# Optimization experiments

Hardware: AMD Instinct MI355X
Metric: run time of the kernel (lower is better)

The kernel has to match this reference:

```python
import jax, jax.numpy as jnp
import numpy as np

B, T, G, M, D = 8, 2048, 2, 1024, 256
ALPHA = -1.0      # config['dist_to_logits_alpha']
TAU = 2.0         # curr_temp = max_temp at init
EPS = 1e-10


def setup_inputs() -> dict:
    key = jax.random.key(0)
    k1, k2, k3 = jax.random.split(key, 3)
    x = jax.random.normal(k1, (B, T, G * D), dtype=jnp.float32)
    # nn.init.uniform_(embedding, -0.999, 0.999)
    embedding = jax.random.uniform(k2, (G, M, D), dtype=jnp.float32, minval=-0.999, maxval=0.999)
    # uniform noise for gumbel sampling, clipped away from {0,1}
    gumbel_u = jax.random.uniform(k3, (B * T, G, M), dtype=jnp.float32, minval=1e-6, maxval=1.0 - 1e-6)
    return {"x": x, "embedding": embedding, "gumbel_u": gumbel_u}


def reference(x, embedding, gumbel_u):
    b, t, c = x.shape
    g, m, d = embedding.shape
    xf = x.reshape(-1, g, d)                                  # [N, G, D]

    sq_e = jnp.sum(embedding ** 2, axis=-1)                   # [G, M]
    sq_x = jnp.sum(xf ** 2, axis=-1, keepdims=True)           # [N, G, 1]
    cross = jnp.einsum('ngd,gmd->ngm', xf, embedding)         # [N, G, M]
    logits = ALPHA * (sq_e[None] + sq_x - 2.0 * cross)        # [N, G, M]

    # hard-assignment code perplexity
    hard_x = jax.nn.one_hot(jnp.argmax(logits, axis=-1), m, dtype=logits.dtype)
    hard_probs = hard_x.mean(axis=0)                          # [G, M]
    code_perplexity = -jnp.sum(hard_probs * jnp.log2(hard_probs + EPS), axis=-1)

    # soft-assignment prob perplexity
    avg_probs = jax.nn.softmax(logits, axis=-1).mean(axis=0)  # [G, M]
    prob_perplexity = -jnp.sum(avg_probs * jnp.log2(avg_probs + EPS), axis=-1)

    # gumbel-softmax (hard=True, straight-through)
    gumbels = -jnp.log(-jnp.log(gumbel_u))
    y_soft = jax.nn.softmax((logits + gumbels) / TAU, axis=-1)
    idx = jnp.argmax(y_soft, axis=-1)                         # [N, G]
    y_hard = jax.nn.one_hot(idx, m, dtype=y_soft.dtype)
    st = y_hard + y_soft - jax.lax.stop_gradient(y_soft)      # straight-through one-hot

    # weighted sum over the codebook (avoids [N, G, M, D] blowup of the original)
    quantized = jnp.einsum('ngm,gmd->ngd', st, embedding).reshape(b, t, c)

    quantization_inds = idx.reshape(b, t, g).astype(jnp.int32)
    # use_vq_loss=True: F.mse_loss(x, quantized.detach())
    commitment_loss = jnp.mean((x - jax.lax.stop_gradient(quantized)) ** 2)

    return quantized, code_perplexity, prob_perplexity, quantization_inds, commitment_loss
```

## Files before the change

### kernel.cpp

```cpp
#include <hip/hip_runtime.h>
#include <math.h>

#define NTOT 16384
#define GG 2
#define MM 1024
#define DD 256

#define OFF_Q  ((size_t)0)
#define OFF_CP ((size_t)8388608)
#define OFF_PP ((size_t)8388610)
#define OFF_I  ((size_t)8388612)
#define OFF_L  ((size_t)8421380)

#define SHIFT 40.0f
#define REFINE_GAP 0.03f

typedef __attribute__((ext_vector_type(8))) short bf16x8;
typedef __attribute__((ext_vector_type(4))) float f32x4;
typedef unsigned short u16;
typedef unsigned int u32;

__device__ inline float wave_sum_f(float v) {
#pragma unroll
  for (int o = 32; o > 0; o >>= 1) v += __shfl_xor(v, o);
  return v;
}
__device__ inline u16 f2bf(float f) {
  u32 u = __float_as_uint(f);
  return (u16)((u + 0x7fffu + ((u >> 16) & 1u)) >> 16);
}
__device__ inline float bf2f(u16 h) {
  return __uint_as_float(((u32)h) << 16);
}
__device__ inline void async16(const void* g, void* l) {
  __builtin_amdgcn_global_load_lds(
      (const __attribute__((address_space(1))) u32*)g,
      (__attribute__((address_space(3))) u32*)l, 16, 0, 0);
}

#define WS_INVZ   32768
#define WS_EHSW   163840
#define WS_ELSW   1212416
#define WS_EST    2260992
#define WS_NEED3  (2260992ull + 2ull * MM * (size_t)NTOT * GG)

__global__ void vq_init2(const float* __restrict__ emb, float* __restrict__ sq_e,
                         float* __restrict__ avg, int* __restrict__ hist,
                         double* __restrict__ loss, u16* __restrict__ eh,
                         u16* __restrict__ el, int do_split) {
  const int row = blockIdx.x * 4 + (threadIdx.x >> 6);
  const int lane = threadIdx.x & 63;
  float4 e4 = *(const float4*)&emb[(size_t)row * DD + lane * 4];
  float s = e4.x * e4.x + e4.y * e4.y + e4.z * e4.z + e4.w * e4.w;
  s = wave_sum_f(s);
  if (do_split) {
    ushort4 h, l;
    h.x = f2bf(e4.x); l.x = f2bf(e4.x - bf2f(h.x));
    h.y = f2bf(e4.y); l.y = f2bf(e4.y - bf2f(h.y));
    h.z = f2bf(e4.z); l.z = f2bf(e4.z - bf2f(h.z));
    h.w = f2bf(e4.w); l.w = f2bf(e4.w - bf2f(h.w));
    *(ushort4*)&eh[(size_t)row * DD + lane * 4] = h;
    *(ushort4*)&el[(size_t)row * DD + lane * 4] = l;
  }
  if (lane == 0) sq_e[row] = s;
  if (blockIdx.x == 0) {
    for (int i = threadIdx.x; i < GG * MM; i += 256) { avg[i] = 0.f; hist[i] = 0; }
    if (threadIdx.x == 0) *loss = 0.0;
  }
}

__global__ void vq_init_swz(const float* __restrict__ emb, u16* __restrict__ eh_sw,
                            u16* __restrict__ el_sw) {
  int tid = blockIdx.x * 256 + threadIdx.x;
  int g = tid >> 15, rem = tid & 32767;
  int col = rem >> 5, kc = rem & 31;
  const float* src = emb + ((size_t)(g * MM + col)) * DD + kc * 8;
  float4 fa = *(const float4*)src;
  float4 fb = *(const float4*)(src + 4);
  float f[8] = {fa.x, fa.y, fa.z, fa.w, fb.x, fb.y, fb.z, fb.w};
  u16 hi[8], lo[8];
#pragma unroll
  for (int j = 0; j < 8; ++j) {
    hi[j] = f2bf(f[j]);
    lo[j] = f2bf(f[j] - bf2f(hi[j]));
  }
  int ct = col >> 6, cg = (col >> 4) & 3, l15 = col & 15;
  int ks = kc >> 2, quad = kc & 3;
  size_t chunk = ((((size_t)g * 16 + ct) * 8 + ks) * 4 + cg) * 64 + quad * 16 + l15;
  ushort4* dh = (ushort4*)(eh_sw + chunk * 8);
  ushort4* dl = (ushort4*)(el_sw + chunk * 8);
  dh[0] = make_ushort4(hi[0], hi[1], hi[2], hi[3]);
  dh[1] = make_ushort4(hi[4], hi[5], hi[6], hi[7]);
  dl[0] = make_ushort4(lo[0], lo[1], lo[2], lo[3]);
  dl[1] = make_ushort4(lo[4], lo[5], lo[6], lo[7]);
}

__global__ __launch_bounds__(256, 2) void vq_main3(
    const float* __restrict__ x, const float* __restrict__ emb,
    const float* __restrict__ gum, const float* __restrict__ sq_e,
    const u16* __restrict__ eh_sw, const u16* __restrict__ el_sw,
    float* __restrict__ out, u16* __restrict__ est, float* __restrict__ invZ_ws,
    int* __restrict__ hist, double* __restrict__ loss) {
  __shared__ u16 bt[2][32768];
  __shared__ int fidx_lds[128];

  const int g = blockIdx.y;
  const int n0 = blockIdx.x * 128;
  const int t = threadIdx.x;
  const int wave = t >> 6, lane = t & 63;
  const int quad = lane >> 4, l15 = lane & 15;
  const int nw = n0 + wave * 32;

  float* xs = (float*)&bt[0][0];
  {
    const float* xb = x + (size_t)nw * (GG * DD) + (size_t)g * DD;
#pragma unroll 4
    for (int j = 0; j < 32; ++j) {
      float4 v = *(const float4*)(xb + (size_t)j * (GG * DD) + lane * 4);
      *(float4*)&xs[wave * 8192 + j * 256 + ((lane ^ (j & 7)) << 2)] = v;
    }
  }
  __syncthreads();

  bf16x8 ah[2][8], al[2][8];
#pragma unroll
  for (int s = 0; s < 2; ++s) {
#pragma unroll
    for (int ks = 0; ks < 8; ++ks) {
      int row = s * 16 + l15;
      int c0 = ks * 8 + quad * 2;
      const float* base = &xs[wave * 8192 + row * 256];
      float4 f0 = *(const float4*)&base[((c0 ^ (row & 7)) << 2)];
      float4 f1 = *(const float4*)&base[(((c0 + 1) ^ (row & 7)) << 2)];
      float f[8] = {f0.x, f0.y, f0.z, f0.w, f1.x, f1.y, f1.z, f1.w};
#pragma unroll
      for (int j = 0; j < 8; ++j) {
        u16 h = f2bf(f[j]);
        ah[s][ks][j] = (short)h;
        al[s][ks][j] = (short)f2bf(f[j] - bf2f(h));
      }
    }
  }
  __syncthreads();

  const u16* sgh = eh_sw + (size_t)g * 16 * 16384;
  const u16* sgl = el_sw + (size_t)g * 16 * 16384;

  auto stage = [&](int ct, int buf) {
    const u16* sh = sgh + (size_t)ct * 16384;
    const u16* sl = sgl + (size_t)ct * 16384;
    u16* dh = &bt[buf][0];
    u16* dl = &bt[buf][16384];
#pragma unroll
    for (int j = 0; j < 8; ++j) {
      int slot = j * 4 + wave;
      async16(sh + slot * 512 + lane * 8, dh + slot * 512);
      async16(sl + slot * 512 + lane * 8, dl + slot * 512);
    }
  };

  float Zl[8], hv[8], z1[8], z2[8];
  int hid[8], i1[8], i2[8];
#pragma unroll
  for (int i = 0; i < 8; ++i) {
    Zl[i] = 0.f; hv[i] = -INFINITY; z1[i] = -INFINITY; z2[i] = -INFINITY;
    hid[i] = 0; i1[i] = 0; i2[i] = 0;
  }

  stage(0, 0);

#pragma unroll 1
  for (int ct = 0; ct < 16; ++ct) {
    __syncthreads();
    if (ct < 15) stage(ct + 1, (ct + 1) & 1);
    const u16* bh_p = &bt[ct & 1][0];
    const u16* bl_p = &bt[ct & 1][16384];
#pragma unroll 1
    for (int cg = 0; cg < 4; ++cg) {
      const int colG = ct * 64 + cg * 16 + l15;
      float sqv = sq_e[g * MM + colG];
      float gv[8];
#pragma unroll
      for (int s = 0; s < 2; ++s)
#pragma unroll
        for (int r = 0; r < 4; ++r)
          gv[s * 4 + r] =
              gum[((size_t)(nw + s * 16 + quad * 4 + r) * GG + g) * MM + colG];

      f32x4 c00 = {0,0,0,0}, c01 = {0,0,0,0}, c02 = {0,0,0,0};
      f32x4 c10 = {0,0,0,0}, c11 = {0,0,0,0}, c12 = {0,0,0,0};
#pragma unroll
      for (int ks = 0; ks < 8; ++ks) {
        int off = ((ks * 4 + cg) * 64 + lane) * 8;
        bf16x8 bh = *(const bf16x8*)(bh_p + off);
        bf16x8 bl = *(const bf16x8*)(bl_p + off);
        c00 = __builtin_amdgcn_mfma_f32_16x16x32_bf16(ah[0][ks], bh, c00, 0, 0, 0);
        c01 = __builtin_amdgcn_mfma_f32_16x16x32_bf16(ah[0][ks], bl, c01, 0, 0, 0);
        c02 = __builtin_amdgcn_mfma_f32_16x16x32_bf16(al[0][ks], bh, c02, 0, 0, 0);
        c10 = __builtin_amdgcn_mfma_f32_16x16x32_bf16(ah[1][ks], bh, c10, 0, 0, 0);
        c11 = __builtin_amdgcn_mfma_f32_16x16x32_bf16(ah[1][ks], bl, c11, 0, 0, 0);
        c12 = __builtin_amdgcn_mfma_f32_16x16x32_bf16(al[1][ks], bh, c12, 0, 0, 0);
      }
#pragma unroll
      for (int s = 0; s < 2; ++s) {
        const f32x4& a0 = s ? c10 : c00;
        const f32x4& a1 = s ? c11 : c01;
        const f32x4& a2 = s ? c12 : c02;
        ushort4 pk;
        u16* pp = (u16*)&pk;
#pragma unroll
        for (int r = 0; r < 4; ++r) {
          float lp = 2.f * (a0[r] + a1[r] + a2[r]) - sqv + SHIFT;
          float ev = expf(fminf(lp, 80.f));
          Zl[s * 4 + r] += ev;
          pp[r] = f2bf(ev);
          if (lp > hv[s * 4 + r]) { hv[s * 4 + r] = lp; hid[s * 4 + r] = colG; }
          float zz = lp - logf(-logf(gv[s * 4 + r]));
          if (zz > z1[s * 4 + r]) {
            z2[s * 4 + r] = z1[s * 4 + r]; i2[s * 4 + r] = i1[s * 4 + r];
            z1[s * 4 + r] = zz; i1[s * 4 + r] = colG;
          } else if (zz > z2[s * 4 + r]) {
            z2[s * 4 + r] = zz; i2[s * 4 + r] = colG;
          }
        }
        *(ushort4*)&est[((size_t)(g * MM + colG) << 14) + nw + s * 16 + quad * 4] = pk;
      }
    }
  }

#pragma unroll 1
  for (int s = 0; s < 2; ++s) {
#pragma unroll 1
    for (int r = 0; r < 4; ++r) {
      const int idx = s * 4 + r;
      const int row = wave * 32 + s * 16 + quad * 4 + r;
      const int n = n0 + row;
      float Zr = Zl[idx], hvr = hv[idx];
      int hir = hid[idx];
      float v1 = z1[idx], v2 = z2[idx];
      int j1 = i1[idx], j2 = i2[idx];
#pragma unroll
      for (int o = 1; o <= 8; o <<= 1) {
        Zr += __shfl_xor(Zr, o);
        float ohv = __shfl_xor(hvr, o); int ohi = __shfl_xor(hir, o);
        if (ohv > hvr || (ohv == hvr && ohi < hir)) { hvr = ohv; hir = ohi; }
        float w1 = __shfl_xor(v1, o), w2 = __shfl_xor(v2, o);
        int k1 = __shfl_xor(j1, o), k2 = __shfl_xor(j2, o);
        if (w1 > v1 || (w1 == v1 && k1 < j1)) {
          if (v1 > w2 || (v1 == w2 && j1 < k2)) { v2 = v1; j2 = j1; }
          else { v2 = w2; j2 = k2; }
          v1 = w1; j1 = k1;
        } else if (w1 > v2 || (w1 == v2 && k1 < j2)) { v2 = w1; j2 = k1; }
      }
      int fidx = j1;
      if (v1 - v2 < REFINE_GAP) {
        const float* xrow = x + (size_t)n * (GG * DD) + (size_t)g * DD;
        const float* eA = emb + ((size_t)g * MM + j1) * DD;
        const float* eB = emb + ((size_t)g * MM + j2) * DD;
        double dA = 0, sA = 0, dB = 0, sB = 0;
#pragma unroll
        for (int k = 0; k < 16; ++k) {
          int d = l15 * 16 + k;
          double xv = (double)xrow[d];
          double ea = (double)eA[d], eb = (double)eB[d];
          dA += xv * ea; sA += ea * ea;
          dB += xv * eb; sB += eb * eb;
        }
#pragma unroll
        for (int o = 1; o <= 8; o <<= 1) {
          dA += __shfl_xor(dA, o); sA += __shfl_xor(sA, o);
          dB += __shfl_xor(dB, o); sB += __shfl_xor(sB, o);
        }
        double uA = (double)gum[((size_t)n * GG + g) * MM + j1];
        double uB = (double)gum[((size_t)n * GG + g) * MM + j2];
        double zA = 2.0 * dA - sA - log(-log(uA));
        double zB = 2.0 * dB - sB - log(-log(uB));
        if (zB > zA || (zB == zA && j2 < j1)) fidx = j2;
      }
      if (l15 == 0) {
        out[OFF_I + (size_t)n * GG + g] = (float)fidx;
        atomicAdd(&hist[g * MM + hir], 1);
        invZ_ws[g * NTOT + n] = 1.f / Zr;
        fidx_lds[row] = fidx;
      }
    }
  }
  __syncthreads();

  {
    float ls = 0.f;
#pragma unroll 4
    for (int j = 0; j < 32; ++j) {
      int idx = j * 256 + t;
      int row = idx >> 6, f4 = idx & 63;
      int n = n0 + row, fi = fidx_lds[row];
      float4 e4 = *(const float4*)&emb[((size_t)g * MM + fi) * DD + f4 * 4];
      float4 x4 = *(const float4*)&x[(size_t)n * (GG * DD) + (size_t)g * DD + f4 * 4];
      *(float4*)&out[OFF_Q + (size_t)n * (GG * DD) + (size_t)g * DD + f4 * 4] = e4;
      float dx = x4.x - e4.x, dy = x4.y - e4.y, dz = x4.z - e4.z, dw = x4.w - e4.w;
      ls += dx * dx + dy * dy + dz * dz + dw * dw;
    }
    ls = wave_sum_f(ls);
    if (lane == 0) atomicAdd(loss, (double)ls);
  }
}

__global__ void vq_avg(const u16* __restrict__ est, const float* __restrict__ invZ,
                       float* __restrict__ avg) {
  int wid = blockIdx.x * 4 + (threadIdx.x >> 6);
  int lane = threadIdx.x & 63;
  const u16* base = est + ((size_t)wid << 14);
  const float* zp = invZ + ((wid >> 10) << 14);
  float acc = 0.f;
#pragma unroll 4
  for (int it = 0; it < 64; ++it) {
    int n = it * 256 + lane * 4;
    ushort4 e4 = *(const ushort4*)(base + n);
    float4 z4 = *(const float4*)(zp + n);
    acc += bf2f(e4.x) * z4.x + bf2f(e4.y) * z4.y +
           bf2f(e4.z) * z4.z + bf2f(e4.w) * z4.w;
  }
  acc = wave_sum_f(acc);
  if (lane == 0) avg[wid] = acc;
}

__global__ void vq_fin(const float* __restrict__ avg, const int* __restrict__ hist,
                       const double* __restrict__ loss, float* __restrict__ out) {
  int g = blockIdx.x, t = threadIdx.x;
  float cp = 0.f, pp = 0.f;
  for (int m = t; m < MM; m += 256) {
    float hp = (float)hist[g * MM + m] * (1.f / 16384.f);
    cp += hp * log2f(hp + 1e-10f);
    float ap = avg[g * MM + m] * (1.f / 16384.f);
    pp += ap * log2f(ap + 1e-10f);
  }
  cp = wave_sum_f(cp);
  pp = wave_sum_f(pp);
  __shared__ float sc[4], sp[4];
  int wave = t >> 6, lane = t & 63;
  if (lane == 0) { sc[wave] = cp; sp[wave] = pp; }
  __syncthreads();
  if (t == 0) {
    out[OFF_CP + g] = -(sc[0] + sc[1] + sc[2] + sc[3]);
    out[OFF_PP + g] = -(sp[0] + sp[1] + sp[2] + sp[3]);
    if (g == 0) out[OFF_L] = (float)(*loss * (1.0 / 8388608.0));
  }
}

__global__ __launch_bounds__(256, 3) void vq_main_fast(
    const float* __restrict__ x, const float* __restrict__ emb,
    const float* __restrict__ gum, const float* __restrict__ sq_e,
    const u16* __restrict__ eh, const u16* __restrict__ el,
    float* __restrict__ out, float* __restrict__ avg,
    int* __restrict__ hist, double* __restrict__ loss) {
  __shared__ u16 est_lds[4][16][264];
  __shared__ float colsum[MM];
  __shared__ float red[16][4][8];
  __shared__ float fin_invZ[16];
  __shared__ int fin_idx[16];

  const int g = blockIdx.y;
  const int n0 = blockIdx.x * 16;
  const int t = threadIdx.x;
  const int wave = t >> 6, lane = t & 63;
  const int quad = lane >> 4, l15 = lane & 15;
  const int wm0 = wave * 256;

  for (int i = t; i < MM; i += 256) colsum[i] = 0.f;

  bf16x8 ah[8], al[8];
  {
    const float* xr = x + (size_t)(n0 + l15) * (GG * DD) + (size_t)g * DD + quad * 8;
#pragma unroll
    for (int ks = 0; ks < 8; ++ks) {
      float4 fa = *(const float4*)(xr + ks * 32);
      float4 fb = *(const float4*)(xr + ks * 32 + 4);
      float f[8] = {fa.x, fa.y, fa.z, fa.w, fb.x, fb.y, fb.z, fb.w};
#pragma unroll
      for (int j = 0; j < 8; ++j) {
        u16 h = f2bf(f[j]);
        ah[ks][j] = (short)h;
        al[ks][j] = (short)f2bf(f[j] - bf2f(h));
      }
    }
  }
  const u16* ehb = eh + ((size_t)g * MM + wm0 + l15) * DD + quad * 8;
  const u16* elb = el + ((size_t)g * MM + wm0 + l15) * DD + quad * 8;
  const float* sqb = sq_e + g * MM + wm0 + l15;

  float Z[4] = {0.f, 0.f, 0.f, 0.f};
  float hv[4] = {-INFINITY, -INFINITY, -INFINITY, -INFINITY};
  int hid[4] = {0, 0, 0, 0};
  float z1[4] = {-INFINITY, -INFINITY, -INFINITY, -INFINITY};
  float z2[4] = {-INFINITY, -INFINITY, -INFINITY, -INFINITY};
  int i1[4] = {0, 0, 0, 0}, i2[4] = {0, 0, 0, 0};

#pragma unroll 2
  for (int tt = 0; tt < 16; ++tt) {
    float sqv = sqb[tt * 16];
    float gv[4];
#pragma unroll
    for (int r = 0; r < 4; ++r)
      gv[r] = gum[((size_t)(n0 + quad * 4 + r) * GG + g) * MM + wm0 + tt * 16 + l15];
    f32x4 a0 = {0,0,0,0}, a1 = {0,0,0,0}, a2 = {0,0,0,0};
#pragma unroll
    for (int ks = 0; ks < 8; ++ks) {
      bf16x8 bh = *(const bf16x8*)(ehb + (size_t)tt * 16 * DD + ks * 32);
      bf16x8 bl = *(const bf16x8*)(elb + (size_t)tt * 16 * DD + ks * 32);
      a0 = __builtin_amdgcn_mfma_f32_16x16x32_bf16(ah[ks], bh, a0, 0, 0, 0);
      a1 = __builtin_amdgcn_mfma_f32_16x16x32_bf16(ah[ks], bl, a1, 0, 0, 0);
      a2 = __builtin_amdgcn_mfma_f32_16x16x32_bf16(al[ks], bh, a2, 0, 0, 0);
    }
    const int colL = tt * 16 + l15;
    const int colG = wm0 + colL;
#pragma unroll
    for (int r = 0; r < 4; ++r) {
      float lp = 2.f * (a0[r] + a1[r] + a2[r]) - sqv + SHIFT;
      float ev = expf(fminf(lp, 80.f));
      Z[r] += ev;
      est_lds[wave][quad * 4 + r][colL] = f2bf(ev);
      if (lp > hv[r]) { hv[r] = lp; hid[r] = colG; }
      float zz = lp - logf(-logf(gv[r]));
      if (zz > z1[r]) { z2[r] = z1[r]; i2[r] = i1[r]; z1[r] = zz; i1[r] = colG; }
      else if (zz > z2[r]) { z2[r] = zz; i2[r] = colG; }
    }
  }
#pragma unroll
  for (int r = 0; r < 4; ++r) {
    float Zr = Z[r], hvr = hv[r];
    int hir = hid[r];
    float v1 = z1[r], v2 = z2[r];
    int j1 = i1[r], j2 = i2[r];
#pragma unroll
    for (int o = 1; o <= 8; o <<= 1) {
      Zr += __shfl_xor(Zr, o);
      float ohv = __shfl_xor(hvr, o); int ohi = __shfl_xor(hir, o);
      if (ohv > hvr || (ohv == hvr && ohi < hir)) { hvr = ohv; hir = ohi; }
      float w1 = __shfl_xor(v1, o), w2 = __shfl_xor(v2, o);
      int k1 = __shfl_xor(j1, o), k2 = __shfl_xor(j2, o);
      if (w1 > v1 || (w1 == v1 && k1 < j1)) {
        if (v1 > w2 || (v1 == w2 && j1 < k2)) { v2 = v1; j2 = j1; }
        else { v2 = w2; j2 = k2; }
        v1 = w1; j1 = k1;
      } else if (w1 > v2 || (w1 == v2 && k1 < j2)) { v2 = w1; j2 = k1; }
    }
    if (l15 == 0) {
      float* rp = red[quad * 4 + r][wave];
      rp[0] = Zr; rp[1] = hvr; rp[2] = __int_as_float(hir);
      rp[3] = v1; rp[4] = __int_as_float(j1);
      rp[5] = v2; rp[6] = __int_as_float(j2);
    }
  }
  __syncthreads();
  if (t < 16) {
    const int row = t, n = n0 + row;
    float Zf = 0.f, hvf = -INFINITY; int hif = 0;
    float v1 = -INFINITY, v2 = -INFINITY; int j1 = 0, j2 = 0;
    for (int w = 0; w < 4; ++w) {
      const float* rp = red[row][w];
      Zf += rp[0];
      float ohv = rp[1]; int ohi = __float_as_int(rp[2]);
      if (ohv > hvf || (ohv == hvf && ohi < hif)) { hvf = ohv; hif = ohi; }
      float w1 = rp[3], w2 = rp[5];
      int k1 = __float_as_int(rp[4]), k2 = __float_as_int(rp[6]);
      if (w1 > v1 || (w1 == v1 && k1 < j1)) {
        if (v1 > w2 || (v1 == w2 && j1 < k2)) { v2 = v1; j2 = j1; }
        else { v2 = w2; j2 = k2; }
        v1 = w1; j1 = k1;
      } else if (w1 > v2 || (w1 == v2 && k1 < j2)) { v2 = w1; j2 = k1; }
    }
    int fidx = j1;
    if (v1 - v2 < REFINE_GAP) {
      const float* xrow = x + (size_t)n * (GG * DD) + (size_t)g * DD;
      const float* eA = emb + ((size_t)g * MM + j1) * DD;
      const float* eB = emb + ((size_t)g * MM + j2) * DD;
      double dA = 0, sA = 0, dB = 0, sB = 0;
      for (int d = 0; d < DD; ++d) {
        double xv = xrow[d], ea = eA[d], eb = eB[d];
        dA += xv * ea; sA += ea * ea;
        dB += xv * eb; sB += eb * eb;
      }
      double uA = gum[((size_t)n * GG + g) * MM + j1];
      double uB = gum[((size_t)n * GG + g) * MM + j2];
      double zA = 2.0 * dA - sA - log(-log(uA));
      double zB = 2.0 * dB - sB - log(-log(uB));
      if (zB > zA || (zB == zA && j2 < j1)) fidx = j2;
    }
    out[OFF_I + (size_t)n * GG + g] = (float)fidx;
    atomicAdd(&hist[g * MM + hif], 1);
    fin_invZ[row] = 1.f / Zf;
    fin_idx[row] = fidx;
  }
  __syncthreads();
  {
    const int row = t >> 4, c = (t & 15) * 16;
    const int n = n0 + row, fidx = fin_idx[row];
    const float* er = emb + ((size_t)g * MM + fidx) * DD + c;
    const float* xq = x + (size_t)n * (GG * DD) + (size_t)g * DD + c;
    float* op = out + OFF_Q + (size_t)n * (GG * DD) + (size_t)g * DD + c;
    float ls = 0.f;
#pragma unroll
    for (int j = 0; j < 4; ++j) {
      float4 e4 = *(const float4*)(er + j * 4);
      float4 x4 = *(const float4*)(xq + j * 4);
      *(float4*)(op + j * 4) = e4;
      float dx = x4.x - e4.x, dy = x4.y - e4.y, dz = x4.z - e4.z, dw = x4.w - e4.w;
      ls += dx * dx + dy * dy + dz * dz + dw * dw;
    }
    ls = wave_sum_f(ls);
    if (lane == 0) atomicAdd(loss, (double)ls);
  }
  float iZ[4];
#pragma unroll
  for (int r = 0; r < 4; ++r) iZ[r] = fin_invZ[quad * 4 + r];
#pragma unroll 1
  for (int tt = 0; tt < 16; ++tt) {
    float v = 0.f;
#pragma unroll
    for (int r = 0; r < 4; ++r)
      v += bf2f(est_lds[wave][quad * 4 + r][tt * 16 + l15]) * iZ[r];
    v += __shfl_xor(v, 16);
    v += __shfl_xor(v, 32);
    if (lane < 16) colsum[wm0 + tt * 16 + lane] += v;
  }
  __syncthreads();
  for (int i = t; i < MM; i += 256) atomicAdd(&avg[g * MM + i], colsum[i]);
}

extern "C" void kernel_launch(void* const* d_in, const int* in_sizes, int n_in,
                              void* d_out, int out_size, void* d_ws, size_t ws_size,
                              hipStream_t stream) {
  const float* x = (const float*)d_in[0];
  const float* emb = (const float*)d_in[1];
  const float* gum = (const float*)d_in[2];
  float* out = (float*)d_out;

  float* sq_e = (float*)d_ws;
  float* avg = (float*)((char*)d_ws + 8192);
  int* hist = (int*)((char*)d_ws + 16384);
  double* loss = (double*)((char*)d_ws + 24576);

  if (ws_size >= WS_NEED3) {
    float* invZ = (float*)((char*)d_ws + WS_INVZ);
    u16* eh_sw = (u16*)((char*)d_ws + WS_EHSW);
    u16* el_sw = (u16*)((char*)d_ws + WS_ELSW);
    u16* est = (u16*)((char*)d_ws + WS_EST);
    vq_init2<<<512, 256, 0, stream>>>(emb, sq_e, avg, hist, loss, eh_sw, el_sw, 0);
    vq_init_swz<<<256, 256, 0, stream>>>(emb, eh_sw, el_sw);
    vq_main3<<<dim3(NTOT / 128, GG), 256, 0, stream>>>(
        x, emb, gum, sq_e, eh_sw, el_sw, out, est, invZ, hist, loss);
    vq_avg<<<512, 256, 0, stream>>>(est, invZ, avg);
    vq_fin<<<GG, 256, 0, stream>>>(avg, hist, loss, out);
  } else {
    u16* eh = (u16*)((char*)d_ws + 32768);
    u16* el = eh + (size_t)GG * MM * DD;
    vq_init2<<<512, 256, 0, stream>>>(emb, sq_e, avg, hist, loss, eh, el, 1);
    vq_main_fast<<<dim3(NTOT / 16, GG), 256, 0, stream>>>(
        x, emb, gum, sq_e, eh, el, out, avg, hist, loss);
    vq_fin<<<GG, 256, 0, stream>>>(avg, hist, loss, out);
  }
}
```

Baseline: 401.0 us.

## Halve codebook LDS tile, load x directly, use fast exp/log intrinsics

The codebook tile staged in LDS shrinks from 64 to 32 columns per step, which halves shared memory per block and doubles the number of stage iterations. The swizzled layout and the stage loop are changed to match. The x rows are now read straight from global memory into bf16 hi/lo fragments instead of going through a swizzled LDS staging pass, which also removes a barrier. Gumbel, est and sq_e base pointers are hoisted out of the loop, expf/logf become __expf/__logf, and the vq_avg loop is widened to 8 elements per lane. The fallback path for small workspaces is deleted, so the code now assumes the workspace is large enough, and the fast intrinsics may slightly change argmax tie cases.

New measurement: 577.6 us. 44.0% more time.

```diff
diff --git a/kernel.cpp b/kernel.cpp
--- a/kernel.cpp
+++ b/kernel.cpp
@@ -42,26 +42,15 @@
 #define WS_EHSW   163840
 #define WS_ELSW   1212416
 #define WS_EST    2260992
-#define WS_NEED3  (2260992ull + 2ull * MM * (size_t)NTOT * GG)
 
 __global__ void vq_init2(const float* __restrict__ emb, float* __restrict__ sq_e,
                          float* __restrict__ avg, int* __restrict__ hist,
-                         double* __restrict__ loss, u16* __restrict__ eh,
-                         u16* __restrict__ el, int do_split) {
+                         double* __restrict__ loss) {
   const int row = blockIdx.x * 4 + (threadIdx.x >> 6);
   const int lane = threadIdx.x & 63;
   float4 e4 = *(const float4*)&emb[(size_t)row * DD + lane * 4];
   float s = e4.x * e4.x + e4.y * e4.y + e4.z * e4.z + e4.w * e4.w;
   s = wave_sum_f(s);
-  if (do_split) {
-    ushort4 h, l;
-    h.x = f2bf(e4.x); l.x = f2bf(e4.x - bf2f(h.x));
-    h.y = f2bf(e4.y); l.y = f2bf(e4.y - bf2f(h.y));
-    h.z = f2bf(e4.z); l.z = f2bf(e4.z - bf2f(h.z));
-    h.w = f2bf(e4.w); l.w = f2bf(e4.w - bf2f(h.w));
-    *(ushort4*)&eh[(size_t)row * DD + lane * 4] = h;
-    *(ushort4*)&el[(size_t)row * DD + lane * 4] = l;
-  }
   if (lane == 0) sq_e[row] = s;
   if (blockIdx.x == 0) {
     for (int i = threadIdx.x; i < GG * MM; i += 256) { avg[i] = 0.f; hist[i] = 0; }
@@ -84,9 +73,9 @@
     hi[j] = f2bf(f[j]);
     lo[j] = f2bf(f[j] - bf2f(hi[j]));
   }
-  int ct = col >> 6, cg = (col >> 4) & 3, l15 = col & 15;
+  int ct = col >> 5, cg = (col >> 4) & 1, l15 = col & 15;
   int ks = kc >> 2, quad = kc & 3;
-  size_t chunk = ((((size_t)g * 16 + ct) * 8 + ks) * 4 + cg) * 64 + quad * 16 + l15;
+  size_t chunk = ((((size_t)g * 32 + ct) * 8 + ks) * 2 + cg) * 64 + quad * 16 + l15;
   ushort4* dh = (ushort4*)(eh_sw + chunk * 8);
   ushort4* dl = (ushort4*)(el_sw + chunk * 8);
   dh[0] = make_ushort4(hi[0], hi[1], hi[2], hi[3]);
@@ -95,13 +84,13 @@
   dl[1] = make_ushort4(lo[4], lo[5], lo[6], lo[7]);
 }
 
-__global__ __launch_bounds__(256, 2) void vq_main3(
+__global__ __launch_bounds__(256, 2) void vq_main4(
     const float* __restrict__ x, const float* __restrict__ emb,
     const float* __restrict__ gum, const float* __restrict__ sq_e,
     const u16* __restrict__ eh_sw, const u16* __restrict__ el_sw,
     float* __restrict__ out, u16* __restrict__ est, float* __restrict__ invZ_ws,
     int* __restrict__ hist, double* __restrict__ loss) {
-  __shared__ u16 bt[2][32768];
+  __shared__ u16 bt[2][16384];
   __shared__ int fidx_lds[128];
 
   const int g = blockIdx.y;
@@ -111,28 +100,15 @@
   const int quad = lane >> 4, l15 = lane & 15;
   const int nw = n0 + wave * 32;
 
-  float* xs = (float*)&bt[0][0];
-  {
-    const float* xb = x + (size_t)nw * (GG * DD) + (size_t)g * DD;
-#pragma unroll 4
-    for (int j = 0; j < 32; ++j) {
-      float4 v = *(const float4*)(xb + (size_t)j * (GG * DD) + lane * 4);
-      *(float4*)&xs[wave * 8192 + j * 256 + ((lane ^ (j & 7)) << 2)] = v;
-    }
-  }
-  __syncthreads();
-
   bf16x8 ah[2][8], al[2][8];
 #pragma unroll
   for (int s = 0; s < 2; ++s) {
+    const float* xr = x + (size_t)(nw + s * 16 + l15) * (GG * DD) + (size_t)g * DD + quad * 8;
 #pragma unroll
     for (int ks = 0; ks < 8; ++ks) {
-      int row = s * 16 + l15;
-      int c0 = ks * 8 + quad * 2;
-      const float* base = &xs[wave * 8192 + row * 256];
-      float4 f0 = *(const float4*)&base[((c0 ^ (row & 7)) << 2)];
-      float4 f1 = *(const float4*)&base[(((c0 + 1) ^ (row & 7)) << 2)];
-      float f[8] = {f0.x, f0.y, f0.z, f0.w, f1.x, f1.y, f1.z, f1.w};
+      float4 fa = *(const float4*)(xr + ks * 32);
+      float4 fb = *(const float4*)(xr + ks * 32 + 4);
+      float f[8] = {fa.x, fa.y, fa.z, fa.w, fb.x, fb.y, fb.z, fb.w};
 #pragma unroll
       for (int j = 0; j < 8; ++j) {
         u16 h = f2bf(f[j]);
@@ -141,18 +117,29 @@
       }
     }
   }
-  __syncthreads();
-
-  const u16* sgh = eh_sw + (size_t)g * 16 * 16384;
-  const u16* sgl = el_sw + (size_t)g * 16 * 16384;
+
+  const float* gumb[8];
+  u16* estb[2];
+#pragma unroll
+  for (int s = 0; s < 2; ++s) {
+    estb[s] = est + ((size_t)g * MM << 14) + nw + s * 16 + quad * 4;
+#pragma unroll
+    for (int r = 0; r < 4; ++r)
+      gumb[s * 4 + r] =
+          gum + ((size_t)(nw + s * 16 + quad * 4 + r) * GG + g) * MM;
+  }
+  const float* sqb = sq_e + g * MM + l15;
+
+  const u16* sgh = eh_sw + (size_t)g * 32 * 8192;
+  const u16* sgl = el_sw + (size_t)g * 32 * 8192;
 
   auto stage = [&](int ct, int buf) {
-    const u16* sh = sgh + (size_t)ct * 16384;
-    const u16* sl = sgl + (size_t)ct * 16384;
+    const u16* sh = sgh + (size_t)ct * 8192;
+    const u16* sl = sgl + (size_t)ct * 8192;
     u16* dh = &bt[buf][0];
-    u16* dl = &bt[buf][16384];
-#pragma unroll
-    for (int j = 0; j < 8; ++j) {
+    u16* dl = &bt[buf][8192];
+#pragma unroll
+    for (int j = 0; j < 4; ++j) {
       int slot = j * 4 + wave;
       async16(sh + slot * 512 + lane * 8, dh + slot * 512);
       async16(sl + slot * 512 + lane * 8, dl + slot * 512);
@@ -170,28 +157,24 @@
   stage(0, 0);
 
 #pragma unroll 1
-  for (int ct = 0; ct < 16; ++ct) {
+  for (int ct = 0; ct < 32; ++ct) {
     __syncthreads();
-    if (ct < 15) stage(ct + 1, (ct + 1) & 1);
+    if (ct < 31) stage(ct + 1, (ct + 1) & 1);
     const u16* bh_p = &bt[ct & 1][0];
-    const u16* bl_p = &bt[ct & 1][16384];
+    const u16* bl_p = &bt[ct & 1][8192];
 #pragma unroll 1
-    for (int cg = 0; cg < 4; ++cg) {
-      const int colG = ct * 64 + cg * 16 + l15;
-      float sqv = sq_e[g * MM + colG];
+    for (int cg = 0; cg < 2; ++cg) {
+      const int colG = ct * 32 + cg * 16 + l15;
+      float sqv = sqb[ct * 32 + cg * 16];
       float gv[8];
 #pragma unroll
-      for (int s = 0; s < 2; ++s)
-#pragma unroll
-        for (int r = 0; r < 4; ++r)
-          gv[s * 4 + r] =
-              gum[((size_t)(nw + s * 16 + quad * 4 + r) * GG + g) * MM + colG];
+      for (int i = 0; i < 8; ++i) gv[i] = gumb[i][colG];
 
       f32x4 c00 = {0,0,0,0}, c01 = {0,0,0,0}, c02 = {0,0,0,0};
       f32x4 c10 = {0,0,0,0}, c11 = {0,0,0,0}, c12 = {0,0,0,0};
 #pragma unroll
       for (int ks = 0; ks < 8; ++ks) {
-        int off = ((ks * 4 + cg) * 64 + lane) * 8;
+        int off = ((ks * 2 + cg) * 64 + lane) * 8;
         bf16x8 bh = *(const bf16x8*)(bh_p + off);
         bf16x8 bl = *(const bf16x8*)(bl_p + off);
         c00 = __builtin_amdgcn_mfma_f32_16x16x32_bf16(ah[0][ks], bh, c00, 0, 0, 0);
@@ -211,11 +194,11 @@
 #pragma unroll
         for (int r = 0; r < 4; ++r) {
           float lp = 2.f * (a0[r] + a1[r] + a2[r]) - sqv + SHIFT;
-          float ev = expf(fminf(lp, 80.f));
+          float ev = __expf(fminf(lp, 80.f));
           Zl[s * 4 + r] += ev;
           pp[r] = f2bf(ev);
           if (lp > hv[s * 4 + r]) { hv[s * 4 + r] = lp; hid[s * 4 + r] = colG; }
-          float zz = lp - logf(-logf(gv[s * 4 + r]));
+          float zz = lp - __logf(-__logf(gv[s * 4 + r]));
           if (zz > z1[s * 4 + r]) {
             z2[s * 4 + r] = z1[s * 4 + r]; i2[s * 4 + r] = i1[s * 4 + r];
             z1[s * 4 + r] = zz; i1[s * 4 + r] = colG;
@@ -223,7 +206,7 @@
             z2[s * 4 + r] = zz; i2[s * 4 + r] = colG;
           }
         }
-        *(ushort4*)&est[((size_t)(g * MM + colG) << 14) + nw + s * 16 + quad * 4] = pk;
+        *(ushort4*)(estb[s] + ((size_t)colG << 14)) = pk;
       }
     }
   }
@@ -313,12 +296,16 @@
   const float* zp = invZ + ((wid >> 10) << 14);
   float acc = 0.f;
 #pragma unroll 4
-  for (int it = 0; it < 64; ++it) {
-    int n = it * 256 + lane * 4;
-    ushort4 e4 = *(const ushort4*)(base + n);
-    float4 z4 = *(const float4*)(zp + n);
-    acc += bf2f(e4.x) * z4.x + bf2f(e4.y) * z4.y +
-           bf2f(e4.z) * z4.z + bf2f(e4.w) * z4.w;
+  for (int it = 0; it < 32; ++it) {
+    int n = it * 512 + lane * 8;
+    ushort4 ea = *(const ushort4*)(base + n);
+    ushort4 eb = *(const ushort4*)(base + n + 4);
+    float4 za = *(const float4*)(zp + n);
+    float4 zb = *(const float4*)(zp + n + 4);
+    acc += bf2f(ea.x) * za.x + bf2f(ea.y) * za.y +
+           bf2f(ea.z) * za.z + bf2f(ea.w) * za.w;
+    acc += bf2f(eb.x) * zb.x + bf2f(eb.y) * zb.y +
+           bf2f(eb.z) * zb.z + bf2f(eb.w) * zb.w;
   }
   acc = wave_sum_f(acc);
   if (lane == 0) avg[wid] = acc;
@@ -347,186 +334,6 @@
   }
 }
 
-__global__ __launch_bounds__(256, 3) void vq_main_fast(
-    const float* __restrict__ x, const float* __restrict__ emb,
-    const float* __restrict__ gum, const float* __restrict__ sq_e,
-    const u16* __restrict__ eh, const u16* __restrict__ el,
-    float* __restrict__ out, float* __restrict__ avg,
-    int* __restrict__ hist, double* __restrict__ loss) {
-  __shared__ u16 est_lds[4][16][264];
-  __shared__ float colsum[MM];
-  __shared__ float red[16][4][8];
-  __shared__ float fin_invZ[16];
-  __shared__ int fin_idx[16];
-
-  const int g = blockIdx.y;
-  const int n0 = blockIdx.x * 16;
-  const int t = threadIdx.x;
-  const int wave = t >> 6, lane = t & 63;
-  const int quad = lane >> 4, l15 = lane & 15;
-  const int wm0 = wave * 256;
-
-  for (int i = t; i < MM; i += 256) colsum[i] = 0.f;
-
-  bf16x8 ah[8], al[8];
-  {
-    const float* xr = x + (size_t)(n0 + l15) * (GG * DD) + (size_t)g * DD + quad * 8;
-#pragma unroll
-    for (int ks = 0; ks < 8; ++ks) {
-      float4 fa = *(const float4*)(xr + ks * 32);
-      float4 fb = *(const float4*)(xr + ks * 32 + 4);
-      float f[8] = {fa.x, fa.y, fa.z, fa.w, fb.x, fb.y, fb.z, fb.w};
-#pragma unroll
-      for (int j = 0; j < 8; ++j) {
-        u16 h = f2bf(f[j]);
-        ah[ks][j] = (short)h;
-        al[ks][j] = (short)f2bf(f[j] - bf2f(h));
-      }
-    }
-  }
-  const u16* ehb = eh + ((size_t)g * MM + wm0 + l15) * DD + quad * 8;
-  const u16* elb = el + ((size_t)g * MM + wm0 + l15) * DD + quad * 8;
-  const float* sqb = sq_e + g * MM + wm0 + l15;
-
-  float Z[4] = {0.f, 0.f, 0.f, 0.f};
-  float hv[4] = {-INFINITY, -INFINITY, -INFINITY, -INFINITY};
-  int hid[4] = {0, 0, 0, 0};
-  float z1[4] = {-INFINITY, -INFINITY, -INFINITY, -INFINITY};
-  float z2[4] = {-INFINITY, -INFINITY, -INFINITY, -INFINITY};
-  int i1[4] = {0, 0, 0, 0}, i2[4] = {0, 0, 0, 0};
-
-#pragma unroll 2
-  for (int tt = 0; tt < 16; ++tt) {
-    float sqv = sqb[tt * 16];
-    float gv[4];
-#pragma unroll
-    for (int r = 0; r < 4; ++r)
-      gv[r] = gum[((size_t)(n0 + quad * 4 + r) * GG + g) * MM + wm0 + tt * 16 + l15];
-    f32x4 a0 = {0,0,0,0}, a1 = {0,0,0,0}, a2 = {0,0,0,0};
-#pragma unroll
-    for (int ks = 0; ks < 8; ++ks) {
-      bf16x8 bh = *(const bf16x8*)(ehb + (size_t)tt * 16 * DD + ks * 32);
-      bf16x8 bl = *(const bf16x8*)(elb + (size_t)tt * 16 * DD + ks * 32);
-      a0 = __builtin_amdgcn_mfma_f32_16x16x32_bf16(ah[ks], bh, a0, 0, 0, 0);
-      a1 = __builtin_amdgcn_mfma_f32_16x16x32_bf16(ah[ks], bl, a1, 0, 0, 0);
-      a2 = __builtin_amdgcn_mfma_f32_16x16x32_bf16(al[ks], bh, a2, 0, 0, 0);
-    }
-    const int colL = tt * 16 + l15;
-    const int colG = wm0 + colL;
-#pragma unroll
-    for (int r = 0; r < 4; ++r) {
-      float lp = 2.f * (a0[r] + a1[r] + a2[r]) - sqv + SHIFT;
-      float ev = expf(fminf(lp, 80.f));
-      Z[r] += ev;
-      est_lds[wave][quad * 4 + r][colL] = f2bf(ev);
-      if (lp > hv[r]) { hv[r] = lp; hid[r] = colG; }
-      float zz = lp - logf(-logf(gv[r]));
-      if (zz > z1[r]) { z2[r] = z1[r]; i2[r] = i1[r]; z1[r] = zz; i1[r] = colG; }
-      else if (zz > z2[r]) { z2[r] = zz; i2[r] = colG; }
-    }
-  }
-#pragma unroll
-  for (int r = 0; r < 4; ++r) {
-    float Zr = Z[r], hvr = hv[r];
-    int hir = hid[r];
-    float v1 = z1[r], v2 = z2[r];
-    int j1 = i1[r], j2 = i2[r];
-#pragma unroll
-    for (int o = 1; o <= 8; o <<= 1) {
-      Zr += __shfl_xor(Zr, o);
-      float ohv = __shfl_xor(hvr, o); int ohi = __shfl_xor(hir, o);
-      if (ohv > hvr || (ohv == hvr && ohi < hir)) { hvr = ohv; hir = ohi; }
-      float w1 = __shfl_xor(v1, o), w2 = __shfl_xor(v2, o);
-      int k1 = __shfl_xor(j1, o), k2 = __shfl_xor(j2, o);
-      if (w1 > v1 || (w1 == v1 && k1 < j1)) {
-        if (v1 > w2 || (v1 == w2 && j1 < k2)) { v2 = v1; j2 = j1; }
-        else { v2 = w2; j2 = k2; }
-        v1 = w1; j1 = k1;
-      } else if (w1 > v2 || (w1 == v2 && k1 < j2)) { v2 = w1; j2 = k1; }
-    }
-    if (l15 == 0) {
-      float* rp = red[quad * 4 + r][wave];
-      rp[0] = Zr; rp[1] = hvr; rp[2] = __int_as_float(hir);
-      rp[3] = v1; rp[4] = __int_as_float(j1);
-      rp[5] = v2; rp[6] = __int_as_float(j2);
-    }
-  }
-  __syncthreads();
-  if (t < 16) {
-    const int row = t, n = n0 + row;
-    float Zf = 0.f, hvf = -INFINITY; int hif = 0;
-    float v1 = -INFINITY, v2 = -INFINITY; int j1 = 0, j2 = 0;
-    for (int w = 0; w < 4; ++w) {
-      const float* rp = red[row][w];
-      Zf += rp[0];
-      float ohv = rp[1]; int ohi = __float_as_int(rp[2]);
-      if (ohv > hvf || (ohv == hvf && ohi < hif)) { hvf = ohv; hif = ohi; }
-      float w1 = rp[3], w2 = rp[5];
-      int k1 = __float_as_int(rp[4]), k2 = __float_as_int(rp[6]);
-      if (w1 > v1 || (w1 == v1 && k1 < j1)) {
-        if (v1 > w2 || (v1 == w2 && j1 < k2)) { v2 = v1; j2 = j1; }
-        else { v2 = w2; j2 = k2; }
-        v1 = w1; j1 = k1;
-      } else if (w1 > v2 || (w1 == v2 && k1 < j2)) { v2 = w1; j2 = k1; }
-    }
-    int fidx = j1;
-    if (v1 - v2 < REFINE_GAP) {
-      const float* xrow = x + (size_t)n * (GG * DD) + (size_t)g * DD;
-      const float* eA = emb + ((size_t)g * MM + j1) * DD;
-      const float* eB = emb + ((size_t)g * MM + j2) * DD;
-      double dA = 0, sA = 0, dB = 0, sB = 0;
-      for (int d = 0; d < DD; ++d) {
-        double xv = xrow[d], ea = eA[d], eb = eB[d];
-        dA += xv * ea; sA += ea * ea;
-        dB += xv * eb; sB += eb * eb;
-      }
-      double uA = gum[((size_t)n * GG + g) * MM + j1];
-      double uB = gum[((size_t)n * GG + g) * MM + j2];
-      double zA = 2.0 * dA - sA - log(-log(uA));
-      double zB = 2.0 * dB - sB - log(-log(uB));
-      if (zB > zA || (zB == zA && j2 < j1)) fidx = j2;
-    }
-    out[OFF_I + (size_t)n * GG + g] = (float)fidx;
-    atomicAdd(&hist[g * MM + hif], 1);
-    fin_invZ[row] = 1.f / Zf;
-    fin_idx[row] = fidx;
-  }
-  __syncthreads();
-  {
-    const int row = t >> 4, c = (t & 15) * 16;
-    const int n = n0 + row, fidx = fin_idx[row];
-    const float* er = emb + ((size_t)g * MM + fidx) * DD + c;
-    const float* xq = x + (size_t)n * (GG * DD) + (size_t)g * DD + c;
-    float* op = out + OFF_Q + (size_t)n * (GG * DD) + (size_t)g * DD + c;
-    float ls = 0.f;
-#pragma unroll
-    for (int j = 0; j < 4; ++j) {
-      float4 e4 = *(const float4*)(er + j * 4);
-      float4 x4 = *(const float4*)(xq + j * 4);
-      *(float4*)(op + j * 4) = e4;
-      float dx = x4.x - e4.x, dy = x4.y - e4.y, dz = x4.z - e4.z, dw = x4.w - e4.w;
-      ls += dx * dx + dy * dy + dz * dz + dw * dw;
-    }
-    ls = wave_sum_f(ls);
-    if (lane == 0) atomicAdd(loss, (double)ls);
-  }
-  float iZ[4];
-#pragma unroll
-  for (int r = 0; r < 4; ++r) iZ[r] = fin_invZ[quad * 4 + r];
-#pragma unroll 1
-  for (int tt = 0; tt < 16; ++tt) {
-    float v = 0.f;
-#pragma unroll
-    for (int r = 0; r < 4; ++r)
-      v += bf2f(est_lds[wave][quad * 4 + r][tt * 16 + l15]) * iZ[r];
-    v += __shfl_xor(v, 16);
-    v += __shfl_xor(v, 32);
-    if (lane < 16) colsum[wm0 + tt * 16 + lane] += v;
-  }
-  __syncthreads();
-  for (int i = t; i < MM; i += 256) atomicAdd(&avg[g * MM + i], colsum[i]);
-}
-
 extern "C" void kernel_launch(void* const* d_in, const int* in_sizes, int n_in,
                               void* d_out, int out_size, void* d_ws, size_t ws_size,
                               hipStream_t stream) {
@@ -539,24 +346,15 @@
   float* avg = (float*)((char*)d_ws + 8192);
   int* hist = (int*)((char*)d_ws + 16384);
   double* loss = (double*)((char*)d_ws + 24576);
-
-  if (ws_size >= WS_NEED3) {
-    float* invZ = (float*)((char*)d_ws + WS_INVZ);
-    u16* eh_sw = (u16*)((char*)d_ws + WS_EHSW);
-    u16* el_sw = (u16*)((char*)d_ws + WS_ELSW);
-    u16* est = (u16*)((char*)d_ws + WS_EST);
-    vq_init2<<<512, 256, 0, stream>>>(emb, sq_e, avg, hist, loss, eh_sw, el_sw, 0);
-    vq_init_swz<<<256, 256, 0, stream>>>(emb, eh_sw, el_sw);
-    vq_main3<<<dim3(NTOT / 128, GG), 256, 0, stream>>>(
-        x, emb, gum, sq_e, eh_sw, el_sw, out, est, invZ, hist, loss);
-    vq_avg<<<512, 256, 0, stream>>>(est, invZ, avg);
-    vq_fin<<<GG, 256, 0, stream>>>(avg, hist, loss, out);
-  } else {
-    u16* eh = (u16*)((char*)d_ws + 32768);
-    u16* el = eh + (size_t)GG * MM * DD;
-    vq_init2<<<512, 256, 0, stream>>>(emb, sq_e, avg, hist, loss, eh, el, 1);
-    vq_main_fast<<<dim3(NTOT / 16, GG), 256, 0, stream>>>(
-        x, emb, gum, sq_e, eh, el, out, avg, hist, loss);
-    vq_fin<<<GG, 256, 0, stream>>>(avg, hist, loss, out);
-  }
-}
+  float* invZ = (float*)((char*)d_ws + WS_INVZ);
+  u16* eh_sw = (u16*)((char*)d_ws + WS_EHSW);
+  u16* el_sw = (u16*)((char*)d_ws + WS_ELSW);
+  u16* est = (u16*)((char*)d_ws + WS_EST);
+
+  vq_init2<<<512, 256, 0, stream>>>(emb, sq_e, avg, hist, loss);
+  vq_init_swz<<<256, 256, 0, stream>>>(emb, eh_sw, el_sw);
+  vq_main4<<<dim3(NTOT / 128, GG), 256, 0, stream>>>(
+      x, emb, gum, sq_e, eh_sw, el_sw, out, est, invZ, hist, loss);
+  vq_avg<<<512, 256, 0, stream>>>(est, invZ, avg);
+  vq_fin<<<GG, 256, 0, stream>>>(avg, hist, loss, out);
+}
```
